# Kernel optimization log

Hardware: AMD Instinct MI355X
Metric: run time of the kernel (lower is better)

The kernel has to match this reference:

```python
import jax, jax.numpy as jnp
import numpy as np

NUM_HEADS = 16
ROPE_THETA = 10000.0


def _vision_rope_tables(seq_len, head_dim):
    # Llama4 vision ('mllama4') 2D rotary: x/y patch-grid positions,
    # interleaved (non-neox) complex pairs. Returns cos/sin [S, head_dim//2].
    idx = int(np.sqrt(seq_len))  # patches per side (24 for 336/14)
    pos = np.arange(seq_len)
    fx = (pos % idx + 1).astype(np.float32)
    fy = (pos // idx + 1).astype(np.float32)
    freq_dim = head_dim // 2
    rope_freq = 1.0 / ROPE_THETA ** (
        np.arange(0, freq_dim, 2)[: freq_dim // 2].astype(np.float32) / freq_dim
    )
    fx = np.repeat(fx[:, None] * rope_freq[None, :], 2, axis=-1)  # [S, freq_dim]
    fy = np.repeat(fy[:, None] * rope_freq[None, :], 2, axis=-1)
    freqs = np.concatenate([fx, fy], axis=-1)[:, ::2]  # [S, head_dim//2]
    return jnp.asarray(np.cos(freqs)), jnp.asarray(np.sin(freqs))


def _apply_rope(x, cos, sin):
    # x: [B, S, H, D]; even/odd interleaved pairs treated as complex numbers
    B, S, H, D = x.shape
    xr = x.reshape(B, S, H, D // 2, 2)
    x0, x1 = xr[..., 0], xr[..., 1]
    c = cos[None, :, None, :]
    s = sin[None, :, None, :]
    o0 = x0 * c - x1 * s
    o1 = x0 * s + x1 * c
    return jnp.stack([o0, o1], axis=-1).reshape(B, S, H, D)


def setup_inputs() -> dict:
    key = jax.random.key(0)
    ks = jax.random.split(key, 5)
    E = 1408
    B, S = 16, 576
    scale = 0.02
    return {
        "hidden_states": jax.random.normal(ks[0], (B, S, E), dtype=jnp.float32),
        "w_qkv": jax.random.normal(ks[1], (E, 3 * E), dtype=jnp.float32) * scale,
        "b_qkv": jax.random.normal(ks[2], (3 * E,), dtype=jnp.float32) * scale,
        "w_o": jax.random.normal(ks[3], (E, E), dtype=jnp.float32) * scale,
        "b_o": jax.random.normal(ks[4], (E,), dtype=jnp.float32) * scale,
    }


def reference(hidden_states, w_qkv, b_qkv, w_o, b_o):
    B, S, E = hidden_states.shape
    H = NUM_HEADS
    D = E // H
    scaling = D ** -0.5

    qkv = hidden_states @ w_qkv + b_qkv  # [B,S,3E]
    q, k, v = jnp.split(qkv, 3, axis=-1)
    q = q.reshape(B, S, H, D)
    k = k.reshape(B, S, H, D)
    v = v.reshape(B, S, H, D)

    cos, sin = _vision_rope_tables(S, D)
    q = _apply_rope(q, cos, sin)
    k = _apply_rope(k, cos, sin)

    q = q * scaling
    scores = jnp.einsum("bqhd,bkhd->bhqk", q, k)  # full bidirectional attention
    probs = jax.nn.softmax(scores, axis=-1)
    attn = jnp.einsum("bhqk,bkhd->bqhd", probs, v).reshape(B, S, E)

    return attn @ w_o + b_o
```

## Files before the change

### kernel.cpp

```cpp
#include <hip/hip_runtime.h>
#include <hip/hip_bf16.h>


typedef unsigned short UST;
typedef __attribute__((ext_vector_type(8))) __bf16 bf16x8;
typedef __attribute__((ext_vector_type(4))) float f32x4;
typedef __attribute__((ext_vector_type(8))) UST us8;
typedef __attribute__((ext_vector_type(4))) UST us4;

typedef __attribute__((address_space(3))) unsigned int lds_u32;
typedef const __attribute__((address_space(1))) unsigned int glob_u32;

static __device__ __forceinline__ float bf2f(UST u){
  unsigned int x = ((unsigned int)u) << 16;
  return __builtin_bit_cast(float, x);
}
static __device__ __forceinline__ UST f2bf(float f){
  unsigned int x = __builtin_bit_cast(unsigned int, f);
  x += 0x7fffu + ((x >> 16) & 1u);
  return (UST)(x >> 16);
}

__global__ void k_tables(float* __restrict__ cosT, float* __restrict__ sinT){
  int s = blockIdx.x;
  int p = threadIdx.x;
  if (p >= 44) return;
  int tt = p % 22;
  double comp = (p < 22) ? (double)(s % 24 + 1) : (double)(s / 24 + 1);
  double a = comp * pow(10000.0, -(double)tt / 22.0);
  cosT[s*44 + p] = (float)cos(a);
  sinT[s*44 + p] = (float)sin(a);
}

__global__ void k_cvt(const float* __restrict__ in, UST* __restrict__ out, int n4){
  int i = blockIdx.x * 256 + threadIdx.x;
  if (i >= n4) return;
  float4 v = ((const float4*)in)[i];
  us4 o; o[0]=f2bf(v.x); o[1]=f2bf(v.y); o[2]=f2bf(v.z); o[3]=f2bf(v.w);
  *(us4*)(out + 4*(size_t)i) = o;
}

__global__ void k_cvt_t(const float* __restrict__ W, UST* __restrict__ Bt, int K, int N){
  __shared__ __align__(16) UST tl[64][70];
  int kt = blockIdx.x, nt = blockIdx.y;
  int t = threadIdx.x;
  int k = t >> 2, u = t & 3;
  const float* src = W + (size_t)(kt*64 + k)*N + nt*64 + u*16;
#pragma unroll
  for (int i = 0; i < 4; ++i){
    float4 v = *(const float4*)(src + 4*i);
    UST* d = &tl[k][u*16 + 4*i];
    d[0]=f2bf(v.x); d[1]=f2bf(v.y); d[2]=f2bf(v.z); d[3]=f2bf(v.w);
  }
  __syncthreads();
  int n = t >> 2;
  UST* dst = Bt + (size_t)(nt*64 + n)*K + kt*64 + u*16;
#pragma unroll
  for (int i = 0; i < 2; ++i){
    us8 o;
#pragma unroll
    for (int j = 0; j < 8; ++j) o[j] = tl[u*16 + 8*i + j][n];
    *(us8*)(dst + 8*i) = o;
  }
}

template<bool OUT_BF16>
__global__ __launch_bounds__(256, 2) void k_gemm(
    const UST* __restrict__ A, const UST* __restrict__ Bt,
    const float* __restrict__ bias, void* __restrict__ Cout,
    int M, int N, int K)
{
  __shared__ __align__(16) UST lA[2][128][64];
  __shared__ __align__(16) UST lB[2][128][64];
  const int t = threadIdx.x;
  const int bm = blockIdx.x, bn = blockIdx.y;
  const int wave = t >> 6, lane = t & 63;
  const int lm = lane & 15, g = lane >> 4;
  const int wr = (wave >> 1) << 6, wc = (wave & 1) << 6;
  const int lrow = lane >> 3;
  const int lcol = (((lane & 7) ^ lrow) << 3);
  const UST* Ag = A  + (size_t)(bm*128 + wave*32 + lrow)*K + lcol;
  const UST* Bg = Bt + (size_t)(bn*128 + wave*32 + lrow)*K + lcol;

  f32x4 zero = {0.f,0.f,0.f,0.f};
  f32x4 acc[4][4];
#pragma unroll
  for (int i=0;i<4;++i)
#pragma unroll
    for (int j=0;j<4;++j) acc[i][j] = zero;

  const int nkt = K >> 6;
  auto stage = [&](int kt, int buf){
#pragma unroll
    for (int c = 0; c < 4; ++c){
      __builtin_amdgcn_global_load_lds((glob_u32*)(Ag + (size_t)kt*64 + (size_t)(8*c)*K),
                                       (lds_u32*)(&lA[buf][wave*32 + 8*c][0]), 16, 0, 0);
      __builtin_amdgcn_global_load_lds((glob_u32*)(Bg + (size_t)kt*64 + (size_t)(8*c)*K),
                                       (lds_u32*)(&lB[buf][wave*32 + 8*c][0]), 16, 0, 0);
    }
  };

  stage(0, 0);
  __syncthreads();
  const int swz = (lm & 7) << 3;

  for (int kt = 0; kt < nkt; ++kt){
    const int cur = kt & 1;
    if (kt + 1 < nkt) stage(kt + 1, cur ^ 1);
#pragma unroll
    for (int ks = 0; ks < 2; ++ks){
      bf16x8 af[4], bfv[4];
      const int cb = (ks*32 + g*8) ^ swz;
#pragma unroll
      for (int mf = 0; mf < 4; ++mf)
        af[mf] = __builtin_bit_cast(bf16x8, *(const us8*)&lA[cur][wr + mf*16 + lm][cb]);
#pragma unroll
      for (int nf = 0; nf < 4; ++nf)
        bfv[nf] = __builtin_bit_cast(bf16x8, *(const us8*)&lB[cur][wc + nf*16 + lm][cb]);
#pragma unroll
      for (int mf = 0; mf < 4; ++mf)
#pragma unroll
        for (int nf = 0; nf < 4; ++nf)
          acc[mf][nf] = __builtin_amdgcn_mfma_f32_16x16x32_bf16(af[mf], bfv[nf], acc[mf][nf], 0, 0, 0);
    }
    __syncthreads();
  }

#pragma unroll
  for (int nf = 0; nf < 4; ++nf){
    const int col = bn*128 + wc + nf*16 + lm;
    const float bv = bias[col];
#pragma unroll
    for (int mf = 0; mf < 4; ++mf){
      const size_t rb = (size_t)(bm*128 + wr + mf*16 + g*4);
#pragma unroll
      for (int r = 0; r < 4; ++r){
        float v = acc[mf][nf][r] + bv;
        if (OUT_BF16) ((UST*)Cout)[(rb + r)*(size_t)N + col] = f2bf(v);
        else          ((float*)Cout)[(rb + r)*(size_t)N + col] = v;
      }
    }
  }
}

__global__ __launch_bounds__(256) void k_rope(
    const UST* __restrict__ qkv, const float* __restrict__ cosT, const float* __restrict__ sinT,
    UST* __restrict__ qa, UST* __restrict__ ka, UST* __restrict__ vt)
{
  __shared__ float lc[64][44], lsn[64][44];
  __shared__ __align__(16) UST sl[64][104];
  const int bh = blockIdx.x, st = blockIdx.y;
  const int b = bh >> 4, h = bh & 15;
  const int t = threadIdx.x;
  const int s0 = st * 64;
  for (int c = t; c < 64*44; c += 256){
    int s = c / 44, p = c % 44;
    lc[s][p]  = cosT[(s0+s)*44 + p];
    lsn[s][p] = sinT[(s0+s)*44 + p];
  }
  const size_t rowbase = ((size_t)(b*576 + s0))*4224 + h*88;

  for (int j = 0; j < 2; ++j){
    __syncthreads();
    for (int c = t; c < 704; c += 256){
      int r = c / 11, ch = c % 11;
      int chS = (ch < 8) ? (ch ^ ((r>>3)&7)) : ch;
      *(uint4*)&sl[r][chS*8] = *(const uint4*)(qkv + rowbase + (size_t)r*4224 + j*1408 + ch*8);
    }
    __syncthreads();
    const int s = t >> 2, u = t & 3;
    const size_t obase = ((size_t)bh*576 + s0 + s)*96;
    UST* outp = (j == 0) ? qa : ka;
    const float sc = (j == 0) ? 0.10660035817780521f : 1.0f;
    const int sw3 = (s>>3)&7;
#pragma unroll
    for (int i = 0; i < 11; ++i){
      int p = u*11 + i;
      int e = 2*p;
      int chunk = e >> 3;
      int pos = ((chunk < 8) ? (chunk ^ sw3) : chunk)*8 + (e & 7);
      float x0 = bf2f(sl[s][pos]);
      float x1 = bf2f(sl[s][pos+1]);
      float cv = lc[s][p], sv = lsn[s][p];
      float o0 = (x0*cv - x1*sv)*sc;
      float o1 = (x0*sv + x1*cv)*sc;
      unsigned int pk = (unsigned int)f2bf(o0) | ((unsigned int)f2bf(o1) << 16);
      *(unsigned int*)(outp + obase + 2*p) = pk;
    }
    if (u == 3){ uint4 z = {0,0,0,0}; *(uint4*)(outp + obase + 88) = z; }
  }

  __syncthreads();
  for (int c = t; c < 704; c += 256){
    int r = c / 11, ch = c % 11;
    int chS = (ch < 8) ? (ch ^ ((r>>3)&7)) : ch;
    *(uint4*)&sl[r][chS*8] = *(const uint4*)(qkv + rowbase + (size_t)r*4224 + 2*1408 + ch*8);
  }
  __syncthreads();
  for (int c = t; c < 768; c += 256){
    int d = c >> 3, ch = c & 7;
    us8 o;
    if (d < 88){
      int chunk = d >> 3;
#pragma unroll
      for (int jj = 0; jj < 8; ++jj){
        int r = ch*8 + jj;
        int pos = ((chunk < 8) ? (chunk ^ (ch & 7)) : chunk)*8 + (d & 7);
        o[jj] = sl[r][pos];
      }
    } else {
#pragma unroll
      for (int jj = 0; jj < 8; ++jj) o[jj] = 0;
    }
    *(us8*)(vt + ((size_t)bh*96 + d)*576 + s0 + ch*8) = o;
  }
}

__global__ __launch_bounds__(256, 2) void k_attn(
    const UST* __restrict__ qa, const UST* __restrict__ ka,
    const UST* __restrict__ vt, UST* __restrict__ outp)
{
  __shared__ __align__(16) UST lK[64][104];
  __shared__ __align__(16) UST lV[96][72];
  __shared__ __align__(16) UST lP[4][16][72];
  const int bh = blockIdx.x, qt = blockIdx.y;
  const int t = threadIdx.x, wave = t >> 6, lane = t & 63;
  const int lm = lane & 15, g = lane >> 4;
  const int h = bh & 15, b = bh >> 4;

  bf16x8 qf[3];
  {
    const UST* qp = qa + ((size_t)bh*576 + qt*64 + wave*16 + lm)*96 + g*8;
#pragma unroll
    for (int ks = 0; ks < 3; ++ks) qf[ks] = __builtin_bit_cast(bf16x8, *(const us8*)(qp + ks*32));
  }
  f32x4 zero = {0.f,0.f,0.f,0.f};
  f32x4 acc[6];
#pragma unroll
  for (int i = 0; i < 6; ++i) acc[i] = zero;
  float mrun[4], lrun[4];
#pragma unroll
  for (int r = 0; r < 4; ++r){ mrun[r] = -1e30f; lrun[r] = 0.f; }

  const UST* kbase = ka + (size_t)bh*576*96;
  const UST* vbase = vt + (size_t)bh*96*576;

  for (int kvt = 0; kvt < 9; ++kvt){
    {
      int r = t >> 2, u = t & 3;
      const UST* src = kbase + (size_t)(kvt*64 + r)*96 + u*24;
#pragma unroll
      for (int i = 0; i < 3; ++i)
        *(uint4*)&lK[r][u*24 + i*8] = *(const uint4*)(src + i*8);
    }
    if (t < 192){
      int d = t >> 1, hf = t & 1;
      const UST* src = vbase + (size_t)d*576 + kvt*64 + hf*32;
#pragma unroll
      for (int i = 0; i < 4; ++i)
        *(uint4*)&lV[d][hf*32 + i*8] = *(const uint4*)(src + i*8);
    }
    __syncthreads();

    f32x4 sc[4];
#pragma unroll
    for (int i = 0; i < 4; ++i) sc[i] = zero;
#pragma unroll
    for (int ks = 0; ks < 3; ++ks){
#pragma unroll
      for (int nf = 0; nf < 4; ++nf){
        bf16x8 kf = __builtin_bit_cast(bf16x8, *(const us8*)&lK[nf*16 + lm][ks*32 + g*8]);
        sc[nf] = __builtin_amdgcn_mfma_f32_16x16x32_bf16(qf[ks], kf, sc[nf], 0, 0, 0);
      }
    }
    float mx[4];
#pragma unroll
    for (int r = 0; r < 4; ++r)
      mx[r] = fmaxf(fmaxf(sc[0][r], sc[1][r]), fmaxf(sc[2][r], sc[3][r]));
#pragma unroll
    for (int m = 1; m <= 8; m <<= 1)
#pragma unroll
      for (int r = 0; r < 4; ++r) mx[r] = fmaxf(mx[r], __shfl_xor(mx[r], m, 64));
    float al[4];
#pragma unroll
    for (int r = 0; r < 4; ++r){
      float mnew = fmaxf(mrun[r], mx[r]);
      float corr = __expf(mrun[r] - mnew);
      mrun[r] = mnew;
      lrun[r] *= corr;
      float ls = 0.f;
#pragma unroll
      for (int nf = 0; nf < 4; ++nf){
        float p = __expf(sc[nf][r] - mnew);
        sc[nf][r] = p;
        ls += p;
      }
#pragma unroll
      for (int df = 0; df < 6; ++df) acc[df][r] *= corr;
      al[r] = ls;
    }
#pragma unroll
    for (int m = 1; m <= 8; m <<= 1)
#pragma unroll
      for (int r = 0; r < 4; ++r) al[r] += __shfl_xor(al[r], m, 64);
#pragma unroll
    for (int r = 0; r < 4; ++r) lrun[r] += al[r];

#pragma unroll
    for (int nf = 0; nf < 4; ++nf)
#pragma unroll
      for (int r = 0; r < 4; ++r)
        lP[wave][4*g + r][nf*16 + lm] = f2bf(sc[nf][r]);

    bf16x8 pa[2];
#pragma unroll
    for (int ks2 = 0; ks2 < 2; ++ks2)
      pa[ks2] = __builtin_bit_cast(bf16x8, *(const us8*)&lP[wave][lm][ks2*32 + g*8]);
#pragma unroll
    for (int ks2 = 0; ks2 < 2; ++ks2)
#pragma unroll
      for (int df = 0; df < 6; ++df){
        bf16x8 vf = __builtin_bit_cast(bf16x8, *(const us8*)&lV[df*16 + lm][ks2*32 + g*8]);
        acc[df] = __builtin_amdgcn_mfma_f32_16x16x32_bf16(pa[ks2], vf, acc[df], 0, 0, 0);
      }
    __syncthreads();
  }

  float inv[4];
#pragma unroll
  for (int r = 0; r < 4; ++r) inv[r] = 1.f / lrun[r];
  const size_t rowt = (size_t)b*576 + qt*64 + wave*16;
#pragma unroll
  for (int df = 0; df < 6; ++df){
    int d = df*16 + lm;
    if (d < 88){
#pragma unroll
      for (int r = 0; r < 4; ++r)
        outp[(rowt + 4*g + r)*1408 + h*88 + d] = f2bf(acc[df][r] * inv[r]);
    }
  }
}

extern "C" void kernel_launch(void* const* d_in, const int* in_sizes, int n_in,
                              void* d_out, int out_size, void* d_ws, size_t ws_size,
                              hipStream_t stream)
{
  (void)in_sizes; (void)n_in; (void)out_size; (void)ws_size;
  const float* hs   = (const float*)d_in[0];
  const float* wqkv = (const float*)d_in[1];
  const float* bqkv = (const float*)d_in[2];
  const float* wo   = (const float*)d_in[3];
  const float* bo   = (const float*)d_in[4];
  float* out = (float*)d_out;

  char* w = (char*)d_ws;
  UST* A_bf   = (UST*)(w);
  UST* Bt1    = (UST*)(w + 25952256);
  UST* Bt2    = (UST*)(w + 37847040);
  UST* qkvb   = (UST*)(w + 41811968);
  UST* qa     = (UST*)(w + 119668736);
  UST* ka     = (UST*)(w + 147980288);
  UST* vt     = (UST*)(w + 176291840);
  float* cosT = (float*)(w + 204603392);
  float* sinT = (float*)(w + 204704768);

  k_tables<<<576, 64, 0, stream>>>(cosT, sinT);
  k_cvt<<<12672, 256, 0, stream>>>(hs, A_bf, 3244032);
  k_cvt_t<<<dim3(22, 66), 256, 0, stream>>>(wqkv, Bt1, 1408, 4224);
  k_cvt_t<<<dim3(22, 22), 256, 0, stream>>>(wo, Bt2, 1408, 1408);
  k_gemm<true ><<<dim3(72, 33), 256, 0, stream>>>(A_bf, Bt1, bqkv, qkvb, 9216, 4224, 1408);
  k_rope<<<dim3(256, 9), 256, 0, stream>>>(qkvb, cosT, sinT, qa, ka, vt);
  k_attn<<<dim3(256, 9), 256, 0, stream>>>(qa, ka, vt, A_bf);
  k_gemm<false><<<dim3(72, 11), 256, 0, stream>>>(A_bf, Bt2, bo, out, 9216, 1408, 1408);
}
```

Before: 353.7 us.

## Widen GEMM tiles to 128x256 with 8 waves and half-K pipelined staging

Replaces the 128x128, 4-wave GEMM with a 128x256, 8-wave kernel. The kernel splits each 64-wide K tile into two 32-wide halves and keeps loads in flight across the MFMA phases, using explicit vmcnt waits, barriers and setprio. The weight transpose pads N up to a multiple of 256 by writing zero blocks, and the workspace offsets are shifted to fit. The aim is more reuse of each A tile and deeper overlap of global-to-LDS loads with MFMA work. The cost is padded wasted columns, especially for the 1408-wide output GEMM, and lower occupancy at one block per CU.

```diff
diff --git a/kernel.cpp b/kernel.cpp
--- a/kernel.cpp
+++ b/kernel.cpp
@@ -44,7 +44,15 @@
   __shared__ __align__(16) UST tl[64][70];
   int kt = blockIdx.x, nt = blockIdx.y;
   int t = threadIdx.x;
-  int k = t >> 2, u = t & 3;
+  int u = t & 3;
+  int n = t >> 2;
+  UST* dst = Bt + (size_t)(nt*64 + n)*K + kt*64 + u*16;
+  if (nt*64 >= N){
+    us8 z = {0,0,0,0,0,0,0,0};
+    *(us8*)(dst) = z; *(us8*)(dst + 8) = z;
+    return;
+  }
+  int k = t >> 2;
   const float* src = W + (size_t)(kt*64 + k)*N + nt*64 + u*16;
 #pragma unroll
   for (int i = 0; i < 4; ++i){
@@ -53,8 +61,6 @@
     d[0]=f2bf(v.x); d[1]=f2bf(v.y); d[2]=f2bf(v.z); d[3]=f2bf(v.w);
   }
   __syncthreads();
-  int n = t >> 2;
-  UST* dst = Bt + (size_t)(nt*64 + n)*K + kt*64 + u*16;
 #pragma unroll
   for (int i = 0; i < 2; ++i){
     us8 o;
@@ -65,22 +71,38 @@
 }
 
 template<bool OUT_BF16>
-__global__ __launch_bounds__(256, 2) void k_gemm(
+__global__ __launch_bounds__(512, 1) void k_gemm8(
     const UST* __restrict__ A, const UST* __restrict__ Bt,
     const float* __restrict__ bias, void* __restrict__ Cout,
     int M, int N, int K)
 {
-  __shared__ __align__(16) UST lA[2][128][64];
-  __shared__ __align__(16) UST lB[2][128][64];
+  __shared__ __align__(16) UST lA[2][2][128][32];
+  __shared__ __align__(16) UST lB[2][2][256][32];
   const int t = threadIdx.x;
   const int bm = blockIdx.x, bn = blockIdx.y;
   const int wave = t >> 6, lane = t & 63;
   const int lm = lane & 15, g = lane >> 4;
-  const int wr = (wave >> 1) << 6, wc = (wave & 1) << 6;
-  const int lrow = lane >> 3;
-  const int lcol = (((lane & 7) ^ lrow) << 3);
-  const UST* Ag = A  + (size_t)(bm*128 + wave*32 + lrow)*K + lcol;
-  const UST* Bg = Bt + (size_t)(bn*128 + wave*32 + lrow)*K + lcol;
+  const int wr = wave >> 2, wc = wave & 3;
+
+  const int srow = t >> 2;
+  const int schunk = ((t & 3) ^ ((t >> 3) & 3)) * 8;
+  const UST* Ag  = A  + (size_t)(bm*128 + srow)*K + schunk;
+  const UST* Bg0 = Bt + (size_t)(bn*256 + srow)*K + schunk;
+  const UST* Bg1 = Bt + (size_t)(bn*256 + 128 + srow)*K + schunk;
+
+  const int nkt = K >> 6;
+
+  auto stage = [&](int tt, int kh){
+    if (tt >= nkt) return;
+    const int s = tt & 1;
+    const size_t go = (size_t)(tt*64 + kh*32);
+    __builtin_amdgcn_global_load_lds((glob_u32*)(Ag + go),
+        (lds_u32*)((UST*)&lA[s][kh][0][0] + wave*512), 16, 0, 0);
+    __builtin_amdgcn_global_load_lds((glob_u32*)(Bg0 + go),
+        (lds_u32*)((UST*)&lB[s][kh][0][0] + wave*512), 16, 0, 0);
+    __builtin_amdgcn_global_load_lds((glob_u32*)(Bg1 + go),
+        (lds_u32*)((UST*)&lB[s][kh][0][0] + 4096 + wave*512), 16, 0, 0);
+  };
 
   f32x4 zero = {0.f,0.f,0.f,0.f};
   f32x4 acc[4][4];
@@ -89,50 +111,48 @@
 #pragma unroll
     for (int j=0;j<4;++j) acc[i][j] = zero;
 
-  const int nkt = K >> 6;
-  auto stage = [&](int kt, int buf){
-#pragma unroll
-    for (int c = 0; c < 4; ++c){
-      __builtin_amdgcn_global_load_lds((glob_u32*)(Ag + (size_t)kt*64 + (size_t)(8*c)*K),
-                                       (lds_u32*)(&lA[buf][wave*32 + 8*c][0]), 16, 0, 0);
-      __builtin_amdgcn_global_load_lds((glob_u32*)(Bg + (size_t)kt*64 + (size_t)(8*c)*K),
-                                       (lds_u32*)(&lB[buf][wave*32 + 8*c][0]), 16, 0, 0);
-    }
-  };
-
-  stage(0, 0);
-  __syncthreads();
-  const int swz = (lm & 7) << 3;
-
-  for (int kt = 0; kt < nkt; ++kt){
-    const int cur = kt & 1;
-    if (kt + 1 < nkt) stage(kt + 1, cur ^ 1);
+  stage(0,0); stage(0,1); stage(1,0);
+  asm volatile("s_waitcnt vmcnt(6)" ::: "memory");
+  __builtin_amdgcn_s_barrier();
+
+  const int rsw = (lm >> 1) & 3;
+  const int arow = wr*64 + lm;
+  const int brow = wc*64 + lm;
+
+  for (int tt = 0; tt < nkt; ++tt){
+    const int s = tt & 1;
 #pragma unroll
     for (int ks = 0; ks < 2; ++ks){
       bf16x8 af[4], bfv[4];
-      const int cb = (ks*32 + g*8) ^ swz;
 #pragma unroll
       for (int mf = 0; mf < 4; ++mf)
-        af[mf] = __builtin_bit_cast(bf16x8, *(const us8*)&lA[cur][wr + mf*16 + lm][cb]);
+        af[mf] = __builtin_bit_cast(bf16x8, *(const us8*)&lA[s][ks][arow + mf*16][(g ^ rsw)*8]);
 #pragma unroll
       for (int nf = 0; nf < 4; ++nf)
-        bfv[nf] = __builtin_bit_cast(bf16x8, *(const us8*)&lB[cur][wc + nf*16 + lm][cb]);
+        bfv[nf] = __builtin_bit_cast(bf16x8, *(const us8*)&lB[s][ks][brow + nf*16][(g ^ rsw)*8]);
+      if (ks == 0) stage(tt + 1, 1);
+      else         stage(tt + 2, 0);
+      asm volatile("s_waitcnt vmcnt(6)" ::: "memory");
+      __builtin_amdgcn_s_barrier();
+      __builtin_amdgcn_s_setprio(1);
 #pragma unroll
       for (int mf = 0; mf < 4; ++mf)
 #pragma unroll
         for (int nf = 0; nf < 4; ++nf)
           acc[mf][nf] = __builtin_amdgcn_mfma_f32_16x16x32_bf16(af[mf], bfv[nf], acc[mf][nf], 0, 0, 0);
-    }
-    __syncthreads();
+      __builtin_amdgcn_s_setprio(0);
+      __builtin_amdgcn_s_barrier();
+    }
   }
 
 #pragma unroll
   for (int nf = 0; nf < 4; ++nf){
-    const int col = bn*128 + wc + nf*16 + lm;
+    const int col = bn*256 + wc*64 + nf*16 + lm;
+    if (col >= N) continue;
     const float bv = bias[col];
 #pragma unroll
     for (int mf = 0; mf < 4; ++mf){
-      const size_t rb = (size_t)(bm*128 + wr + mf*16 + g*4);
+      const size_t rb = (size_t)(bm*128 + wr*64 + mf*16 + g*4);
 #pragma unroll
       for (int r = 0; r < 4; ++r){
         float v = acc[mf][nf][r] + bv;
@@ -356,20 +376,20 @@
   char* w = (char*)d_ws;
   UST* A_bf   = (UST*)(w);
   UST* Bt1    = (UST*)(w + 25952256);
-  UST* Bt2    = (UST*)(w + 37847040);
-  UST* qkvb   = (UST*)(w + 41811968);
-  UST* qa     = (UST*)(w + 119668736);
-  UST* ka     = (UST*)(w + 147980288);
-  UST* vt     = (UST*)(w + 176291840);
-  float* cosT = (float*)(w + 204603392);
-  float* sinT = (float*)(w + 204704768);
+  UST* Bt2    = (UST*)(w + 38207488);
+  UST* qkvb   = (UST*)(w + 42532864);
+  UST* qa     = (UST*)(w + 120389632);
+  UST* ka     = (UST*)(w + 148701184);
+  UST* vt     = (UST*)(w + 177012736);
+  float* cosT = (float*)(w + 205324288);
+  float* sinT = (float*)(w + 205425664);
 
   k_tables<<<576, 64, 0, stream>>>(cosT, sinT);
   k_cvt<<<12672, 256, 0, stream>>>(hs, A_bf, 3244032);
-  k_cvt_t<<<dim3(22, 66), 256, 0, stream>>>(wqkv, Bt1, 1408, 4224);
-  k_cvt_t<<<dim3(22, 22), 256, 0, stream>>>(wo, Bt2, 1408, 1408);
-  k_gemm<true ><<<dim3(72, 33), 256, 0, stream>>>(A_bf, Bt1, bqkv, qkvb, 9216, 4224, 1408);
+  k_cvt_t<<<dim3(22, 68), 256, 0, stream>>>(wqkv, Bt1, 1408, 4224);
+  k_cvt_t<<<dim3(22, 24), 256, 0, stream>>>(wo, Bt2, 1408, 1408);
+  k_gemm8<true ><<<dim3(72, 17), 512, 0, stream>>>(A_bf, Bt1, bqkv, qkvb, 9216, 4224, 1408);
   k_rope<<<dim3(256, 9), 256, 0, stream>>>(qkvb, cosT, sinT, qa, ka, vt);
   k_attn<<<dim3(256, 9), 256, 0, stream>>>(qa, ka, vt, A_bf);
-  k_gemm<false><<<dim3(72, 11), 256, 0, stream>>>(A_bf, Bt2, bo, out, 9216, 1408, 1408);
-}
+  k_gemm8<false><<<dim3(72, 6), 512, 0, stream>>>(A_bf, Bt2, bo, out, 9216, 1408, 1408);
+}
```

Result: slower. 373.1 us (+5.5%).

## Double-buffer attention K/V via async LDS loads, XCD-swizzle grids, relax GEMM barriers

Applied to the files above, without the earlier changes.

The attention kernel now stages K and V tiles into double-buffered LDS with async global_load_lds and XOR-swizzled layouts, so the next tile's loads overlap the current tile's MFMAs. Raw s_barrier with explicit vmcnt waits replaces __syncthreads in both the GEMM and attention loops, and s_setprio raises priority around the MFMA sections. Both kernels switch to 1D grids whose block index is remapped so that neighbouring tiles share an XCD for L2 reuse. The trade-offs are manual wait-count bookkeeping that must match the load count, and one redundant wrap-around prefetch per loop.

```diff
diff --git a/kernel.cpp b/kernel.cpp
--- a/kernel.cpp
+++ b/kernel.cpp
@@ -73,7 +73,10 @@
   __shared__ __align__(16) UST lA[2][128][64];
   __shared__ __align__(16) UST lB[2][128][64];
   const int t = threadIdx.x;
-  const int bm = blockIdx.x, bn = blockIdx.y;
+  const int nwg = gridDim.x;
+  const int v = (blockIdx.x & 7) * (nwg >> 3) + (blockIdx.x >> 3);
+  const int mb = M >> 7;
+  const int bm = v % mb, bn = v / mb;
   const int wave = t >> 6, lane = t & 63;
   const int lm = lane & 15, g = lane >> 4;
   const int wr = (wave >> 1) << 6, wc = (wave & 1) << 6;
@@ -101,12 +104,14 @@
   };
 
   stage(0, 0);
-  __syncthreads();
   const int swz = (lm & 7) << 3;
 
   for (int kt = 0; kt < nkt; ++kt){
     const int cur = kt & 1;
-    if (kt + 1 < nkt) stage(kt + 1, cur ^ 1);
+    stage((kt + 1) % nkt, cur ^ 1);
+    asm volatile("s_waitcnt vmcnt(8)" ::: "memory");
+    __builtin_amdgcn_sched_barrier(0);
+    __builtin_amdgcn_s_barrier();
 #pragma unroll
     for (int ks = 0; ks < 2; ++ks){
       bf16x8 af[4], bfv[4];
@@ -123,7 +128,7 @@
         for (int nf = 0; nf < 4; ++nf)
           acc[mf][nf] = __builtin_amdgcn_mfma_f32_16x16x32_bf16(af[mf], bfv[nf], acc[mf][nf], 0, 0, 0);
     }
-    __syncthreads();
+    __builtin_amdgcn_s_barrier();
   }
 
 #pragma unroll
@@ -135,9 +140,9 @@
       const size_t rb = (size_t)(bm*128 + wr + mf*16 + g*4);
 #pragma unroll
       for (int r = 0; r < 4; ++r){
-        float v = acc[mf][nf][r] + bv;
-        if (OUT_BF16) ((UST*)Cout)[(rb + r)*(size_t)N + col] = f2bf(v);
-        else          ((float*)Cout)[(rb + r)*(size_t)N + col] = v;
+        float v2 = acc[mf][nf][r] + bv;
+        if (OUT_BF16) ((UST*)Cout)[(rb + r)*(size_t)N + col] = f2bf(v2);
+        else          ((float*)Cout)[(rb + r)*(size_t)N + col] = v2;
       }
     }
   }
@@ -220,14 +225,40 @@
     const UST* __restrict__ qa, const UST* __restrict__ ka,
     const UST* __restrict__ vt, UST* __restrict__ outp)
 {
-  __shared__ __align__(16) UST lK[64][104];
-  __shared__ __align__(16) UST lV[96][72];
+  __shared__ __align__(16) UST lK[2][64][96];
+  __shared__ __align__(16) UST lV[2][96][64];
   __shared__ __align__(16) UST lP[4][16][72];
-  const int bh = blockIdx.x, qt = blockIdx.y;
+  const int nwg = gridDim.x;
+  const int vswz = (blockIdx.x & 7) * (nwg >> 3) + (blockIdx.x >> 3);
+  const int qt = vswz % 9, bh = vswz / 9;
   const int t = threadIdx.x, wave = t >> 6, lane = t & 63;
   const int lm = lane & 15, g = lane >> 4;
   const int h = bh & 15, b = bh >> 4;
 
+  const UST* kbase = ka + (size_t)bh*576*96;
+  const UST* vbase = vt + (size_t)bh*96*576;
+
+  int koff[3], vofs[3], ldsoff[3];
+#pragma unroll
+  for (int i = 0; i < 3; ++i){
+    int ch = (i*4 + wave)*64 + lane;
+    int rK = ch / 12, pcK = ch % 12;
+    int scK = (pcK < 8) ? (pcK ^ (rK & 7)) : (8 + ((pcK - 8) ^ (rK & 3)));
+    koff[i] = rK*96 + scK*8;
+    int rV = ch >> 3, pcV = ch & 7;
+    vofs[i] = rV*576 + (pcV ^ (rV & 7))*8;
+    ldsoff[i] = (i*4 + wave)*512;
+  }
+  auto stage = [&](int kvt, int buf){
+#pragma unroll
+    for (int i = 0; i < 3; ++i){
+      __builtin_amdgcn_global_load_lds((glob_u32*)(kbase + (size_t)kvt*6144 + koff[i]),
+                                       (lds_u32*)((UST*)&lK[buf][0][0] + ldsoff[i]), 16, 0, 0);
+      __builtin_amdgcn_global_load_lds((glob_u32*)(vbase + (size_t)kvt*64 + vofs[i]),
+                                       (lds_u32*)((UST*)&lV[buf][0][0] + ldsoff[i]), 16, 0, 0);
+    }
+  };
+
   bf16x8 qf[3];
   {
     const UST* qp = qa + ((size_t)bh*576 + qt*64 + wave*16 + lm)*96 + g*8;
@@ -242,37 +273,36 @@
 #pragma unroll
   for (int r = 0; r < 4; ++r){ mrun[r] = -1e30f; lrun[r] = 0.f; }
 
-  const UST* kbase = ka + (size_t)bh*576*96;
-  const UST* vbase = vt + (size_t)bh*96*576;
+  int kcol_r[3], vcol_r[2];
+  kcol_r[0] = ((0*4 + g) ^ (lm & 7)) * 8;
+  kcol_r[1] = ((1*4 + g) ^ (lm & 7)) * 8;
+  kcol_r[2] = (8 + (g ^ (lm & 3))) * 8;
+#pragma unroll
+  for (int ks2 = 0; ks2 < 2; ++ks2) vcol_r[ks2] = ((ks2*4 + g) ^ (lm & 7)) * 8;
+
+  stage(0, 0);
 
   for (int kvt = 0; kvt < 9; ++kvt){
-    {
-      int r = t >> 2, u = t & 3;
-      const UST* src = kbase + (size_t)(kvt*64 + r)*96 + u*24;
-#pragma unroll
-      for (int i = 0; i < 3; ++i)
-        *(uint4*)&lK[r][u*24 + i*8] = *(const uint4*)(src + i*8);
-    }
-    if (t < 192){
-      int d = t >> 1, hf = t & 1;
-      const UST* src = vbase + (size_t)d*576 + kvt*64 + hf*32;
-#pragma unroll
-      for (int i = 0; i < 4; ++i)
-        *(uint4*)&lV[d][hf*32 + i*8] = *(const uint4*)(src + i*8);
-    }
-    __syncthreads();
+    const int cur = kvt & 1;
+    stage((kvt + 1) % 9, cur ^ 1);
+    asm volatile("s_waitcnt vmcnt(6)" ::: "memory");
+    __builtin_amdgcn_sched_barrier(0);
+    __builtin_amdgcn_s_barrier();
 
     f32x4 sc[4];
 #pragma unroll
     for (int i = 0; i < 4; ++i) sc[i] = zero;
+    __builtin_amdgcn_s_setprio(1);
 #pragma unroll
     for (int ks = 0; ks < 3; ++ks){
 #pragma unroll
       for (int nf = 0; nf < 4; ++nf){
-        bf16x8 kf = __builtin_bit_cast(bf16x8, *(const us8*)&lK[nf*16 + lm][ks*32 + g*8]);
+        bf16x8 kf = __builtin_bit_cast(bf16x8, *(const us8*)&lK[cur][nf*16 + lm][kcol_r[ks]]);
         sc[nf] = __builtin_amdgcn_mfma_f32_16x16x32_bf16(qf[ks], kf, sc[nf], 0, 0, 0);
       }
     }
+    __builtin_amdgcn_s_setprio(0);
+
     float mx[4];
 #pragma unroll
     for (int r = 0; r < 4; ++r)
@@ -316,14 +346,16 @@
 #pragma unroll
     for (int ks2 = 0; ks2 < 2; ++ks2)
       pa[ks2] = __builtin_bit_cast(bf16x8, *(const us8*)&lP[wave][lm][ks2*32 + g*8]);
+    __builtin_amdgcn_s_setprio(1);
 #pragma unroll
     for (int ks2 = 0; ks2 < 2; ++ks2)
 #pragma unroll
       for (int df = 0; df < 6; ++df){
-        bf16x8 vf = __builtin_bit_cast(bf16x8, *(const us8*)&lV[df*16 + lm][ks2*32 + g*8]);
+        bf16x8 vf = __builtin_bit_cast(bf16x8, *(const us8*)&lV[cur][df*16 + lm][vcol_r[ks2]]);
         acc[df] = __builtin_amdgcn_mfma_f32_16x16x32_bf16(pa[ks2], vf, acc[df], 0, 0, 0);
       }
-    __syncthreads();
+    __builtin_amdgcn_s_setprio(0);
+    __builtin_amdgcn_s_barrier();
   }
 
   float inv[4];
@@ -368,8 +400,8 @@
   k_cvt<<<12672, 256, 0, stream>>>(hs, A_bf, 3244032);
   k_cvt_t<<<dim3(22, 66), 256, 0, stream>>>(wqkv, Bt1, 1408, 4224);
   k_cvt_t<<<dim3(22, 22), 256, 0, stream>>>(wo, Bt2, 1408, 1408);
-  k_gemm<true ><<<dim3(72, 33), 256, 0, stream>>>(A_bf, Bt1, bqkv, qkvb, 9216, 4224, 1408);
+  k_gemm<true ><<<2376, 256, 0, stream>>>(A_bf, Bt1, bqkv, qkvb, 9216, 4224, 1408);
   k_rope<<<dim3(256, 9), 256, 0, stream>>>(qkvb, cosT, sinT, qa, ka, vt);
-  k_attn<<<dim3(256, 9), 256, 0, stream>>>(qa, ka, vt, A_bf);
-  k_gemm<false><<<dim3(72, 11), 256, 0, stream>>>(A_bf, Bt2, bo, out, 9216, 1408, 1408);
-}
+  k_attn<<<2304, 256, 0, stream>>>(qa, ka, vt, A_bf);
+  k_gemm<false><<<792, 256, 0, stream>>>(A_bf, Bt2, bo, out, 9216, 1408, 1408);
+}
```

New measurement: 386.4 us. 9.3% more time.

## Write V transposed from QKV GEMM epilogue and simplify RoPE kernel

Applied to the files above, without the earlier changes.

Splits the QKV GEMM into a Q/K part writing bf16 rows and a V part whose epilogue writes V directly in the transposed per-head layout the attention kernel consumes. This removes the V round trip and the LDS transpose from the RoPE pass. RoPE becomes a flat elementwise kernel that reads interleaved cos/sin tables and writes q/k rows. A separate zero kernel fills the padded V rows. The cost is one extra launch, and the transposed-V epilogue stores are strided across rows and less coalesced.

```diff
diff --git a/kernel.cpp b/kernel.cpp
--- a/kernel.cpp
+++ b/kernel.cpp
@@ -21,15 +21,22 @@
   return (UST)(x >> 16);
 }
 
-__global__ void k_tables(float* __restrict__ cosT, float* __restrict__ sinT){
+__global__ void k_tables(float* __restrict__ cs2){
   int s = blockIdx.x;
   int p = threadIdx.x;
   if (p >= 44) return;
   int tt = p % 22;
   double comp = (p < 22) ? (double)(s % 24 + 1) : (double)(s / 24 + 1);
   double a = comp * pow(10000.0, -(double)tt / 22.0);
-  cosT[s*44 + p] = (float)cos(a);
-  sinT[s*44 + p] = (float)sin(a);
+  cs2[s*88 + 2*p]     = (float)cos(a);
+  cs2[s*88 + 2*p + 1] = (float)sin(a);
+}
+
+__global__ void k_zero(UST* __restrict__ vt){
+  int c = blockIdx.x*256 + threadIdx.x;
+  int bh = c / 576, w = c - bh*576;
+  us8 z = {0,0,0,0,0,0,0,0};
+  *(us8*)(vt + (size_t)bh*55296 + 50688 + w*8) = z;
 }
 
 __global__ void k_cvt(const float* __restrict__ in, UST* __restrict__ out, int n4){
@@ -64,16 +71,16 @@
   }
 }
 
-template<bool OUT_BF16>
+template<int EPI>
 __global__ __launch_bounds__(256, 2) void k_gemm(
     const UST* __restrict__ A, const UST* __restrict__ Bt,
     const float* __restrict__ bias, void* __restrict__ Cout,
-    int M, int N, int K)
+    int M, int N, int K, int bn0)
 {
   __shared__ __align__(16) UST lA[2][128][64];
   __shared__ __align__(16) UST lB[2][128][64];
   const int t = threadIdx.x;
-  const int bm = blockIdx.x, bn = blockIdx.y;
+  const int bm = blockIdx.x, bn = blockIdx.y + bn0;
   const int wave = t >> 6, lane = t & 63;
   const int lm = lane & 15, g = lane >> 4;
   const int wr = (wave >> 1) << 6, wc = (wave & 1) << 6;
@@ -130,90 +137,65 @@
   for (int nf = 0; nf < 4; ++nf){
     const int col = bn*128 + wc + nf*16 + lm;
     const float bv = bias[col];
-#pragma unroll
-    for (int mf = 0; mf < 4; ++mf){
-      const size_t rb = (size_t)(bm*128 + wr + mf*16 + g*4);
-#pragma unroll
-      for (int r = 0; r < 4; ++r){
-        float v = acc[mf][nf][r] + bv;
-        if (OUT_BF16) ((UST*)Cout)[(rb + r)*(size_t)N + col] = f2bf(v);
-        else          ((float*)Cout)[(rb + r)*(size_t)N + col] = v;
-      }
-    }
-  }
-}
-
-__global__ __launch_bounds__(256) void k_rope(
-    const UST* __restrict__ qkv, const float* __restrict__ cosT, const float* __restrict__ sinT,
-    UST* __restrict__ qa, UST* __restrict__ ka, UST* __restrict__ vt)
+    if (EPI == 2){
+      const int cv = col - 2816;
+      const int h = cv / 88, d = cv - h*88;
+#pragma unroll
+      for (int mf = 0; mf < 4; ++mf){
+        const int rb = bm*128 + wr + mf*16 + g*4;
+        const int b2 = rb / 576, s = rb - b2*576;
+        UST* dst = (UST*)Cout + ((size_t)((b2*16 + h)*96 + d))*576 + s;
+        us4 pk;
+#pragma unroll
+        for (int r = 0; r < 4; ++r) pk[r] = f2bf(acc[mf][nf][r] + bv);
+        *(us4*)dst = pk;
+      }
+    } else {
+#pragma unroll
+      for (int mf = 0; mf < 4; ++mf){
+        const size_t rb = (size_t)(bm*128 + wr + mf*16 + g*4);
+#pragma unroll
+        for (int r = 0; r < 4; ++r){
+          float v2 = acc[mf][nf][r] + bv;
+          if (EPI == 1) ((UST*)Cout)[(rb + r)*(size_t)N + col] = f2bf(v2);
+          else          ((float*)Cout)[(rb + r)*(size_t)N + col] = v2;
+        }
+      }
+    }
+  }
+}
+
+__global__ __launch_bounds__(256) void k_ropelite(
+    const UST* __restrict__ qkvb, const float* __restrict__ cs2,
+    UST* __restrict__ qa, UST* __restrict__ ka)
 {
-  __shared__ float lc[64][44], lsn[64][44];
-  __shared__ __align__(16) UST sl[64][104];
-  const int bh = blockIdx.x, st = blockIdx.y;
-  const int b = bh >> 4, h = bh & 15;
-  const int t = threadIdx.x;
-  const int s0 = st * 64;
-  for (int c = t; c < 64*44; c += 256){
-    int s = c / 44, p = c % 44;
-    lc[s][p]  = cosT[(s0+s)*44 + p];
-    lsn[s][p] = sinT[(s0+s)*44 + p];
-  }
-  const size_t rowbase = ((size_t)(b*576 + s0))*4224 + h*88;
-
-  for (int j = 0; j < 2; ++j){
-    __syncthreads();
-    for (int c = t; c < 704; c += 256){
-      int r = c / 11, ch = c % 11;
-      int chS = (ch < 8) ? (ch ^ ((r>>3)&7)) : ch;
-      *(uint4*)&sl[r][chS*8] = *(const uint4*)(qkv + rowbase + (size_t)r*4224 + j*1408 + ch*8);
-    }
-    __syncthreads();
-    const int s = t >> 2, u = t & 3;
-    const size_t obase = ((size_t)bh*576 + s0 + s)*96;
-    UST* outp = (j == 0) ? qa : ka;
-    const float sc = (j == 0) ? 0.10660035817780521f : 1.0f;
-    const int sw3 = (s>>3)&7;
-#pragma unroll
-    for (int i = 0; i < 11; ++i){
-      int p = u*11 + i;
-      int e = 2*p;
-      int chunk = e >> 3;
-      int pos = ((chunk < 8) ? (chunk ^ sw3) : chunk)*8 + (e & 7);
-      float x0 = bf2f(sl[s][pos]);
-      float x1 = bf2f(sl[s][pos+1]);
-      float cv = lc[s][p], sv = lsn[s][p];
-      float o0 = (x0*cv - x1*sv)*sc;
-      float o1 = (x0*sv + x1*cv)*sc;
-      unsigned int pk = (unsigned int)f2bf(o0) | ((unsigned int)f2bf(o1) << 16);
-      *(unsigned int*)(outp + obase + 2*p) = pk;
-    }
-    if (u == 3){ uint4 z = {0,0,0,0}; *(uint4*)(outp + obase + 88) = z; }
-  }
-
-  __syncthreads();
-  for (int c = t; c < 704; c += 256){
-    int r = c / 11, ch = c % 11;
-    int chS = (ch < 8) ? (ch ^ ((r>>3)&7)) : ch;
-    *(uint4*)&sl[r][chS*8] = *(const uint4*)(qkv + rowbase + (size_t)r*4224 + 2*1408 + ch*8);
-  }
-  __syncthreads();
-  for (int c = t; c < 768; c += 256){
-    int d = c >> 3, ch = c & 7;
-    us8 o;
-    if (d < 88){
-      int chunk = d >> 3;
-#pragma unroll
-      for (int jj = 0; jj < 8; ++jj){
-        int r = ch*8 + jj;
-        int pos = ((chunk < 8) ? (chunk ^ (ch & 7)) : chunk)*8 + (d & 7);
-        o[jj] = sl[r][pos];
-      }
-    } else {
-#pragma unroll
-      for (int jj = 0; jj < 8; ++jj) o[jj] = 0;
-    }
-    *(us8*)(vt + ((size_t)bh*96 + d)*576 + s0 + ch*8) = o;
-  }
+  int c = blockIdx.x*256 + threadIdx.x;
+  const int PER = 256*576*11;
+  int j = (c >= PER);
+  int c2 = c - j*PER;
+  int bh = c2 / (576*11);
+  int rem = c2 - bh*(576*11);
+  int s = rem / 11, ch = rem - s*11;
+  int b = bh >> 4, h = bh & 15;
+
+  us8 v = *(const us8*)(qkvb + ((size_t)(b*576 + s))*2816 + j*1408 + h*88 + ch*8);
+  float4 q0 = *(const float4*)(cs2 + s*88 + ch*8);
+  float4 q1 = *(const float4*)(cs2 + s*88 + ch*8 + 4);
+  const float sc = j ? 1.0f : 0.10660035817780521f;
+
+  float cv[4] = {q0.x, q0.z, q1.x, q1.z};
+  float sv[4] = {q0.y, q0.w, q1.y, q1.w};
+  us8 o;
+#pragma unroll
+  for (int i = 0; i < 4; ++i){
+    float x0 = bf2f(v[2*i]);
+    float x1 = bf2f(v[2*i+1]);
+    o[2*i]   = f2bf((x0*cv[i] - x1*sv[i])*sc);
+    o[2*i+1] = f2bf((x0*sv[i] + x1*cv[i])*sc);
+  }
+  UST* outp = (j ? ka : qa) + ((size_t)bh*576 + s)*96;
+  *(us8*)(outp + ch*8) = o;
+  if (ch == 10){ us8 z = {0,0,0,0,0,0,0,0}; *(us8*)(outp + 88) = z; }
 }
 
 __global__ __launch_bounds__(256, 2) void k_attn(
@@ -358,18 +340,19 @@
   UST* Bt1    = (UST*)(w + 25952256);
   UST* Bt2    = (UST*)(w + 37847040);
   UST* qkvb   = (UST*)(w + 41811968);
-  UST* qa     = (UST*)(w + 119668736);
-  UST* ka     = (UST*)(w + 147980288);
-  UST* vt     = (UST*)(w + 176291840);
-  float* cosT = (float*)(w + 204603392);
-  float* sinT = (float*)(w + 204704768);
-
-  k_tables<<<576, 64, 0, stream>>>(cosT, sinT);
+  UST* qa     = (UST*)(w + 93716480);
+  UST* ka     = (UST*)(w + 122028032);
+  UST* vt     = (UST*)(w + 150339584);
+  float* cs2  = (float*)(w + 178651136);
+
+  k_tables<<<576, 64, 0, stream>>>(cs2);
+  k_zero<<<576, 256, 0, stream>>>(vt);
   k_cvt<<<12672, 256, 0, stream>>>(hs, A_bf, 3244032);
   k_cvt_t<<<dim3(22, 66), 256, 0, stream>>>(wqkv, Bt1, 1408, 4224);
   k_cvt_t<<<dim3(22, 22), 256, 0, stream>>>(wo, Bt2, 1408, 1408);
-  k_gemm<true ><<<dim3(72, 33), 256, 0, stream>>>(A_bf, Bt1, bqkv, qkvb, 9216, 4224, 1408);
-  k_rope<<<dim3(256, 9), 256, 0, stream>>>(qkvb, cosT, sinT, qa, ka, vt);
+  k_gemm<1><<<dim3(72, 22), 256, 0, stream>>>(A_bf, Bt1, bqkv, qkvb, 9216, 2816, 1408, 0);
+  k_gemm<2><<<dim3(72, 11), 256, 0, stream>>>(A_bf, Bt1, bqkv, vt,   9216, 0,    1408, 22);
+  k_ropelite<<<12672, 256, 0, stream>>>(qkvb, cs2, qa, ka);
   k_attn<<<dim3(256, 9), 256, 0, stream>>>(qa, ka, vt, A_bf);
-  k_gemm<false><<<dim3(72, 11), 256, 0, stream>>>(A_bf, Bt2, bo, out, 9216, 1408, 1408);
-}
+  k_gemm<0><<<dim3(72, 11), 256, 0, stream>>>(A_bf, Bt2, bo, out, 9216, 1408, 1408, 0);
+}
```

After: 359.5 us. About the same (+1.6%).
